# Kernel tuning notes

Measured on AMD Instinct MI355X. Metric: run time of the kernel, lower is better.

The kernel has to match this reference:

```python
import jax, jax.numpy as jnp
import numpy as np

N_NODES = 100000
N_EDGES = 3200000
N_FEAT = 128
HIDDEN = 16


def gcn_conv(x, W, b, row, col, ew, n):
    """PyG GCNConv: linear -> add self-loops -> sym deg-norm -> scatter-add -> bias."""
    x = x @ W  # [n, out]
    loop = jnp.arange(n)
    row = jnp.concatenate([row, loop])
    col = jnp.concatenate([col, loop])
    ew = jnp.concatenate([ew, jnp.ones((n,), ew.dtype)])  # self-loop weight 1
    deg = jax.ops.segment_sum(ew, col, num_segments=n)  # in-degree by edge weight
    dinv = jnp.where(deg > 0, jax.lax.rsqrt(deg), 0.0)
    norm = dinv[row] * ew * dinv[col]  # [E+n]
    # gather source features, scale, scatter-add at destinations
    out = jax.ops.segment_sum(x[row] * norm[:, None], col, num_segments=n)
    return out + b


def setup_inputs() -> dict:
    key = jax.random.key(0)
    k = jax.random.split(key, 7)
    x = jax.random.normal(k[0], (N_NODES, N_FEAT), dtype=jnp.float32)
    edge_index = jax.random.randint(k[1], (2, N_EDGES), 0, N_NODES, dtype=jnp.int64)
    edge_weight = jax.random.uniform(k[2], (N_EDGES,), dtype=jnp.float32)
    s1 = 1.0 / np.sqrt(N_FEAT)
    s2 = 1.0 / np.sqrt(HIDDEN)
    W1 = jax.random.uniform(k[3], (N_FEAT, HIDDEN), jnp.float32, -s1, s1)
    b1 = jnp.zeros((HIDDEN,), jnp.float32)
    W2 = jax.random.uniform(k[4], (HIDDEN, 1), jnp.float32, -s2, s2)
    b2 = jnp.zeros((1,), jnp.float32)
    return {"x": x, "edge_index": edge_index, "edge_weight": edge_weight,
            "W1": W1, "b1": b1, "W2": W2, "b2": b2}


def reference(x, edge_index, edge_weight, W1, b1, W2, b2):
    n = x.shape[0]
    row, col = edge_index[0], edge_index[1]
    h = gcn_conv(x, W1, b1, row, col, edge_weight, n)
    h = jax.nn.relu(h)
    h = gcn_conv(h, W2, b2, row, col, edge_weight, n)
    return jax.nn.sigmoid(h)[:, 0].astype(jnp.float32)  # squeeze(1)
```

## Files before the change

### kernel.cpp

```cpp
#include <hip/hip_runtime.h>
#include <hip/hip_fp16.h>
#include <math.h>

#define NNODES 100000
#define NEDGES 3200000
#define NF 128
#define NH 16
#define SB 192
#define NSB 521
#define NBLK 512
#define EPB (NEDGES / NBLK)
#define CAP2 6912
#define XWBLK 391

__device__ __forceinline__ __half2 u2h(unsigned u) { union { unsigned u; __half2 h; } c; c.u = u; return c.h; }
__device__ __forceinline__ unsigned h2u(__half2 h) { union { unsigned u; __half2 h; } c; c.h = h; return c.u; }
__device__ __forceinline__ __half2 shfl_h2(__half2 v, int m) {
    int x = __shfl_xor(*(int*)&v, m);
    return *(__half2*)&x;
}

__global__ void k_histxw(const int* __restrict__ col, unsigned* __restrict__ ghist,
                         const float* __restrict__ x, const float* __restrict__ W1,
                         unsigned* __restrict__ xwh) {
    __shared__ float w[NF * NH];
    __shared__ unsigned h[NSB];
    int t = threadIdx.x, b = blockIdx.x;
    if (b < NBLK) {
        for (int i = t; i < NSB; i += 256) h[i] = 0u;
        __syncthreads();
        const int2* c2 = (const int2*)(col + b * EPB);
        for (int i = t; i < EPB / 2; i += 256) {
            int2 c = c2[i];
            atomicAdd(&h[(unsigned)c.x / SB], 1u);
            atomicAdd(&h[(unsigned)c.y / SB], 1u);
        }
        __syncthreads();
        for (int i = t; i < NSB; i += 256) ghist[(size_t)b * NSB + i] = h[i];
    } else {
        for (int i = t; i < NF * NH; i += 256) w[i] = W1[i];
        __syncthreads();
        int i = (b - NBLK) * 256 + t;
        if (i >= NNODES) return;
        float acc[NH];
#pragma unroll
        for (int f = 0; f < NH; ++f) acc[f] = 0.f;
        const float4* xr = (const float4*)(x + (long long)i * NF);
#pragma unroll 8
        for (int k4 = 0; k4 < NF / 4; ++k4) {
            float4 v = xr[k4];
            const float* wk = &w[k4 * 4 * NH];
#pragma unroll
            for (int f = 0; f < NH; ++f)
                acc[f] += v.x * wk[f] + v.y * wk[NH + f] + v.z * wk[2 * NH + f] + v.w * wk[3 * NH + f];
        }
        unsigned u[8];
#pragma unroll
        for (int j = 0; j < 8; ++j)
            u[j] = h2u(__floats2half2_rn(acc[2 * j], acc[2 * j + 1]));
        uint4* o = (uint4*)(xwh + (size_t)i * 8);
        o[0] = make_uint4(u[0], u[1], u[2], u[3]);
        o[1] = make_uint4(u[4], u[5], u[6], u[7]);
    }
}

__global__ __launch_bounds__(NBLK) void k_scan1(unsigned* __restrict__ ghist,
                                                unsigned* __restrict__ totals) {
    int k = blockIdx.x, t = threadIdx.x;
    __shared__ unsigned s[NBLK];
    unsigned v = ghist[(size_t)t * NSB + k];
    s[t] = v;
    __syncthreads();
    for (int off = 1; off < NBLK; off <<= 1) {
        unsigned x = (t >= off) ? s[t - off] : 0u;
        __syncthreads();
        s[t] += x;
        __syncthreads();
    }
    ghist[(size_t)t * NSB + k] = s[t] - v;
    if (t == NBLK - 1) totals[k] = s[t];
}

__global__ __launch_bounds__(512) void k_scatB1(
        const int* __restrict__ row, const int* __restrict__ col,
        const float* __restrict__ ew,
        const unsigned* __restrict__ ghist, const unsigned* __restrict__ totals,
        uint2* __restrict__ spack, unsigned* __restrict__ sbase_out) {
    __shared__ uint2 stage[EPB];
    __shared__ unsigned short sbArr[EPB];
    __shared__ unsigned lcnt[NSB];
    __shared__ unsigned gdelta[NSB];
    __shared__ unsigned scn[512];
    int t = threadIdx.x, b = blockIdx.x;
    int e0 = b * EPB;
    for (int i = t; i < NSB; i += 512) lcnt[i] = 0u;
    __syncthreads();
    const int2* c2 = (const int2*)(col + e0);
    for (int i = t; i < EPB / 2; i += 512) {
        int2 c = c2[i];
        atomicAdd(&lcnt[(unsigned)c.x / SB], 1u);
        atomicAdd(&lcnt[(unsigned)c.y / SB], 1u);
    }
    __syncthreads();
    unsigned tv[2];
    unsigned tp = 0;
#pragma unroll
    for (int j = 0; j < 2; ++j) {
        int i = t * 2 + j;
        tv[j] = (i < NSB) ? totals[i] : 0u;
        tp += tv[j];
    }
    scn[t] = tp;
    __syncthreads();
    for (int off = 1; off < 512; off <<= 1) {
        unsigned x = (t >= off) ? scn[t - off] : 0u;
        __syncthreads();
        scn[t] += x;
        __syncthreads();
    }
    unsigned trun = scn[t] - tp;
    unsigned sb_[2];
#pragma unroll
    for (int j = 0; j < 2; ++j) { sb_[j] = trun; trun += tv[j]; }
    __syncthreads();
    unsigned v[2];
    unsigned p = 0;
#pragma unroll
    for (int j = 0; j < 2; ++j) {
        int i = t * 2 + j;
        v[j] = (i < NSB) ? lcnt[i] : 0u;
        p += v[j];
    }
    scn[t] = p;
    __syncthreads();
    for (int off = 1; off < 512; off <<= 1) {
        unsigned x = (t >= off) ? scn[t - off] : 0u;
        __syncthreads();
        scn[t] += x;
        __syncthreads();
    }
    unsigned run = scn[t] - p;
    __syncthreads();
    unsigned lst[2];
#pragma unroll
    for (int j = 0; j < 2; ++j) {
        int i = t * 2 + j;
        if (i < NSB) {
            lst[j] = run;
            gdelta[i] = sb_[j] + ghist[(size_t)b * NSB + i] - run;
        }
        run += v[j];
    }
    __syncthreads();
#pragma unroll
    for (int j = 0; j < 2; ++j) {
        int i = t * 2 + j;
        if (i < NSB) lcnt[i] = lst[j];
    }
    if (b == 0) {
#pragma unroll
        for (int j = 0; j < 2; ++j) {
            int i = t * 2 + j;
            if (i < NSB) sbase_out[i] = sb_[j];
        }
        if (t == 0) sbase_out[NSB] = NEDGES;
    }
    __syncthreads();
    const int2* r2 = (const int2*)(row + e0);
    const float2* w2 = (const float2*)(ew + e0);
    for (int i = t; i < EPB / 2; i += 512) {
        int2 rr = r2[i];
        int2 cc = c2[i];
        float2 ww = w2[i];
        unsigned sb = (unsigned)cc.x / SB;
        unsigned ln = (unsigned)cc.x - sb * SB;
        unsigned pos = atomicAdd(&lcnt[sb], 1u);
        stage[pos] = make_uint2((unsigned)rr.x | (ln << 17), __float_as_uint(ww.x));
        sbArr[pos] = (unsigned short)sb;
        sb = (unsigned)cc.y / SB;
        ln = (unsigned)cc.y - sb * SB;
        pos = atomicAdd(&lcnt[sb], 1u);
        stage[pos] = make_uint2((unsigned)rr.y | (ln << 17), __float_as_uint(ww.y));
        sbArr[pos] = (unsigned short)sb;
    }
    __syncthreads();
    for (int i = t; i < EPB; i += 512)
        spack[i + gdelta[sbArr[i]]] = stage[i];
}

__global__ __launch_bounds__(512) void k_degdinv(
        const uint2* __restrict__ spack, const unsigned* __restrict__ sbase,
        unsigned* __restrict__ start, float* __restrict__ dinv) {
    __shared__ unsigned hist[SB];
    __shared__ float wdeg[SB];
    __shared__ unsigned scn[512];
    int k = blockIdx.x, t = threadIdx.x;
    unsigned e0 = sbase[k], e1 = sbase[k + 1];
    int ne = (int)(e1 - e0);
    if (t < SB) { hist[t] = 0u; wdeg[t] = 0.f; }
    __syncthreads();
    for (int i = t; i < ne; i += 512) {
        uint2 p = spack[e0 + i];
        unsigned ln = p.x >> 17;
        atomicAdd(&hist[ln], 1u);
        atomicAdd(&wdeg[ln], __uint_as_float(p.y));
    }
    __syncthreads();
    unsigned v = (t < SB) ? hist[t] : 0u;
    scn[t] = v;
    __syncthreads();
    for (int off = 1; off < 512; off <<= 1) {
        unsigned x = (t >= off) ? scn[t - off] : 0u;
        __syncthreads();
        scn[t] += x;
        __syncthreads();
    }
    unsigned excl = scn[t] - v;
    int g = k * SB + t;
    if (t < SB && g < NNODES) {
        start[g] = e0 + excl;
        dinv[g] = rsqrtf(wdeg[t] + 1.0f);
    }
}

__global__ __launch_bounds__(1024) void k_sedge1(
        const uint2* __restrict__ spack, const unsigned* __restrict__ sbase,
        const unsigned* __restrict__ start, const unsigned* __restrict__ xwh,
        const float* __restrict__ dinv, const float* __restrict__ b1,
        const float* __restrict__ W2, float* __restrict__ zn) {
    __shared__ uint2 ed[CAP2];
    __shared__ unsigned lcnt[SB];
    int k = blockIdx.x, t = threadIdx.x;
    unsigned e0 = sbase[k], e1 = sbase[k + 1];
    int ne = (int)(e1 - e0);
    if (t < SB) {
        int g = k * SB + t;
        lcnt[t] = (g < NNODES) ? (start[g] - e0) : (unsigned)ne;
    }
    __syncthreads();
    for (int i = t; i < ne; i += 1024) {
        uint2 p = spack[e0 + i];
        unsigned ln = p.x >> 17;
        unsigned r = p.x & 0x1FFFFu;
        float wd = __uint_as_float(p.y) * dinv[r];
        unsigned pos = atomicAdd(&lcnt[ln], 1u);
        ed[pos] = make_uint2(r, h2u(__float2half2_rn(wd)));
    }
    __syncthreads();
    int wave = t >> 6, lane = t & 63;
    int fg = lane & 3, e4 = lane >> 2;
#pragma unroll
    for (int j = 0; j < SB / 16; ++j) {
        int ln = wave * (SB / 16) + j;
        int g = k * SB + ln;
        if (g >= NNODES) break;
        unsigned o0 = (ln == 0) ? 0u : lcnt[ln - 1];
        unsigned o1 = lcnt[ln];
        __half2 a0 = __float2half2_rn(0.f), a1 = a0;
        for (unsigned e = o0 + e4; e < o1; e += 16) {
            uint2 d = ed[e];
            uint2 q = *(const uint2*)(xwh + (size_t)d.x * 8 + fg * 2);
            a0 = __hfma2(u2h(q.x), u2h(d.y), a0);
            a1 = __hfma2(u2h(q.y), u2h(d.y), a1);
        }
#pragma unroll
        for (int m = 4; m < 64; m <<= 1) {
            a0 = __hadd2(a0, shfl_h2(a0, m));
            a1 = __hadd2(a1, shfl_h2(a1, m));
        }
        float di = dinv[g];
        uint2 qs = *(const uint2*)(xwh + (size_t)g * 8 + fg * 2);
        float ax = __low2float(a0)  + di * __low2float(u2h(qs.x));
        float ay = __high2float(a0) + di * __high2float(u2h(qs.x));
        float az = __low2float(a1)  + di * __low2float(u2h(qs.y));
        float aw = __high2float(a1) + di * __high2float(u2h(qs.y));
        float4 b4 = ((const float4*)b1)[fg];
        float4 w4 = ((const float4*)W2)[fg];
        float s = fmaxf(di * ax + b4.x, 0.f) * w4.x
                + fmaxf(di * ay + b4.y, 0.f) * w4.y
                + fmaxf(di * az + b4.z, 0.f) * w4.z
                + fmaxf(di * aw + b4.w, 0.f) * w4.w;
        s += __shfl_xor(s, 1);
        s += __shfl_xor(s, 2);
        if (lane == 0) zn[g] = s * di;
    }
}

__global__ __launch_bounds__(512) void k_edge2acc(
        const uint2* __restrict__ spack, const unsigned* __restrict__ sbase,
        const float* __restrict__ zn, const float* __restrict__ dinv,
        const float* __restrict__ b2, float* __restrict__ out) {
    __shared__ float zacc[SB];
    int k = blockIdx.x, t = threadIdx.x;
    if (t < SB) zacc[t] = 0.f;
    __syncthreads();
    unsigned e0 = sbase[k], e1 = sbase[k + 1];
    for (unsigned e = e0 + t; e < e1; e += 512) {
        uint2 p = spack[e];
        atomicAdd(&zacc[p.x >> 17], zn[p.x & 0x1FFFFu] * __uint_as_float(p.y));
    }
    __syncthreads();
    int g = k * SB + t;
    if (t < SB && g < NNODES) {
        float di = dinv[g];
        float v = di * zacc[t] + di * zn[g] + b2[0];
        out[g] = 1.f / (1.f + expf(-v));
    }
}

extern "C" void kernel_launch(void* const* d_in, const int* in_sizes, int n_in,
                              void* d_out, int out_size, void* d_ws, size_t ws_size,
                              hipStream_t stream) {
    const float* x  = (const float*)d_in[0];
    const int* eidx = (const int*)d_in[1];
    const float* ew = (const float*)d_in[2];
    const float* W1 = (const float*)d_in[3];
    const float* b1 = (const float*)d_in[4];
    const float* W2 = (const float*)d_in[5];
    const float* b2 = (const float*)d_in[6];
    float* out = (float*)d_out;

    const int* row = eidx;
    const int* col = eidx + NEDGES;

    unsigned* ws = (unsigned*)d_ws;
    uint2*    spack  = (uint2*)ws;
    unsigned* xwh    = ws + 6400000;
    float*    dinv   = (float*)(ws + 7200000);
    float*    zn     = (float*)(ws + 7300000);
    unsigned* start  = ws + 7400000;
    unsigned* sbase  = ws + 7500000;
    unsigned* totals = ws + 7500522;
    unsigned* ghist  = ws + 7501043;

    k_histxw <<<NBLK + XWBLK, 256, 0, stream>>>(col, ghist, x, W1, xwh);
    k_scan1  <<<NSB, NBLK, 0, stream>>>(ghist, totals);
    k_scatB1 <<<NBLK, 512, 0, stream>>>(row, col, ew, ghist, totals, spack, sbase);
    k_degdinv<<<NSB, 512, 0, stream>>>(spack, sbase, start, dinv);
    k_sedge1 <<<NSB, 1024, 0, stream>>>(spack, sbase, start, xwh, dinv, b1, W2, zn);
    k_edge2acc<<<NSB, 512, 0, stream>>>(spack, sbase, zn, dinv, b2, out);
}
```

Before: 145.9 us.

## Store bucketed edges as split row/fp16-weight arrays and prescale XW by dinv

```diff
diff --git a/kernel.cpp b/kernel.cpp
--- a/kernel.cpp
+++ b/kernel.cpp
@@ -19,6 +19,9 @@
     int x = __shfl_xor(*(int*)&v, m);
     return *(__half2*)&x;
 }
+__device__ __forceinline__ unsigned f2h(float f) {
+    return h2u(__floats2half2_rn(f, 0.f)) & 0xffffu;
+}
 
 __global__ void k_histxw(const int* __restrict__ col, unsigned* __restrict__ ghist,
                          const float* __restrict__ x, const float* __restrict__ W1,
@@ -85,8 +88,10 @@
         const int* __restrict__ row, const int* __restrict__ col,
         const float* __restrict__ ew,
         const unsigned* __restrict__ ghist, const unsigned* __restrict__ totals,
-        uint2* __restrict__ spack, unsigned* __restrict__ sbase_out) {
-    __shared__ uint2 stage[EPB];
+        unsigned* __restrict__ brow, unsigned short* __restrict__ bw,
+        unsigned* __restrict__ sbase_out) {
+    __shared__ unsigned stage_row[EPB];
+    __shared__ unsigned short stage_w[EPB];
     __shared__ unsigned short sbArr[EPB];
     __shared__ unsigned lcnt[NSB];
     __shared__ unsigned gdelta[NSB];
@@ -175,41 +180,49 @@
         unsigned sb = (unsigned)cc.x / SB;
         unsigned ln = (unsigned)cc.x - sb * SB;
         unsigned pos = atomicAdd(&lcnt[sb], 1u);
-        stage[pos] = make_uint2((unsigned)rr.x | (ln << 17), __float_as_uint(ww.x));
+        stage_row[pos] = (unsigned)rr.x | (ln << 17);
+        stage_w[pos] = (unsigned short)f2h(ww.x);
         sbArr[pos] = (unsigned short)sb;
         sb = (unsigned)cc.y / SB;
         ln = (unsigned)cc.y - sb * SB;
         pos = atomicAdd(&lcnt[sb], 1u);
-        stage[pos] = make_uint2((unsigned)rr.y | (ln << 17), __float_as_uint(ww.y));
+        stage_row[pos] = (unsigned)rr.y | (ln << 17);
+        stage_w[pos] = (unsigned short)f2h(ww.y);
         sbArr[pos] = (unsigned short)sb;
     }
     __syncthreads();
-    for (int i = t; i < EPB; i += 512)
-        spack[i + gdelta[sbArr[i]]] = stage[i];
-}
-
-__global__ __launch_bounds__(512) void k_degdinv(
-        const uint2* __restrict__ spack, const unsigned* __restrict__ sbase,
-        unsigned* __restrict__ start, float* __restrict__ dinv) {
+    for (int i = t; i < EPB; i += 512) {
+        unsigned pos = i + gdelta[sbArr[i]];
+        brow[pos] = stage_row[i];
+        bw[pos] = stage_w[i];
+    }
+}
+
+__global__ __launch_bounds__(1024) void k_degdinv(
+        const unsigned* __restrict__ brow, const unsigned short* __restrict__ bw,
+        const unsigned* __restrict__ sbase,
+        unsigned* __restrict__ start, float* __restrict__ dinv,
+        const unsigned* __restrict__ xwh, unsigned* __restrict__ xwn) {
     __shared__ unsigned hist[SB];
     __shared__ float wdeg[SB];
-    __shared__ unsigned scn[512];
+    __shared__ unsigned scn[1024];
     int k = blockIdx.x, t = threadIdx.x;
     unsigned e0 = sbase[k], e1 = sbase[k + 1];
     int ne = (int)(e1 - e0);
     if (t < SB) { hist[t] = 0u; wdeg[t] = 0.f; }
     __syncthreads();
-    for (int i = t; i < ne; i += 512) {
-        uint2 p = spack[e0 + i];
-        unsigned ln = p.x >> 17;
+    for (int i = t; i < ne; i += 1024) {
+        unsigned p = brow[e0 + i];
+        unsigned wu = bw[e0 + i];
+        unsigned ln = p >> 17;
         atomicAdd(&hist[ln], 1u);
-        atomicAdd(&wdeg[ln], __uint_as_float(p.y));
+        atomicAdd(&wdeg[ln], __low2float(u2h(wu)));
     }
     __syncthreads();
     unsigned v = (t < SB) ? hist[t] : 0u;
     scn[t] = v;
     __syncthreads();
-    for (int off = 1; off < 512; off <<= 1) {
+    for (int off = 1; off < 1024; off <<= 1) {
         unsigned x = (t >= off) ? scn[t - off] : 0u;
         __syncthreads();
         scn[t] += x;
@@ -219,16 +232,34 @@
     int g = k * SB + t;
     if (t < SB && g < NNODES) {
         start[g] = e0 + excl;
-        dinv[g] = rsqrtf(wdeg[t] + 1.0f);
+        float di = rsqrtf(wdeg[t] + 1.0f);
+        dinv[g] = di;
+        __half2 d2 = __float2half2_rn(di);
+        const uint4* xi = (const uint4*)(xwh + (size_t)g * 8);
+        uint4 A = xi[0], B = xi[1];
+        uint4 o0, o1;
+        o0.x = h2u(__hmul2(u2h(A.x), d2));
+        o0.y = h2u(__hmul2(u2h(A.y), d2));
+        o0.z = h2u(__hmul2(u2h(A.z), d2));
+        o0.w = h2u(__hmul2(u2h(A.w), d2));
+        o1.x = h2u(__hmul2(u2h(B.x), d2));
+        o1.y = h2u(__hmul2(u2h(B.y), d2));
+        o1.z = h2u(__hmul2(u2h(B.z), d2));
+        o1.w = h2u(__hmul2(u2h(B.w), d2));
+        uint4* o = (uint4*)(xwn + (size_t)g * 8);
+        o[0] = o0;
+        o[1] = o1;
     }
 }
 
 __global__ __launch_bounds__(1024) void k_sedge1(
-        const uint2* __restrict__ spack, const unsigned* __restrict__ sbase,
-        const unsigned* __restrict__ start, const unsigned* __restrict__ xwh,
+        const unsigned* __restrict__ brow, const unsigned short* __restrict__ bw,
+        const unsigned* __restrict__ sbase,
+        const unsigned* __restrict__ start, const unsigned* __restrict__ xwn,
         const float* __restrict__ dinv, const float* __restrict__ b1,
         const float* __restrict__ W2, float* __restrict__ zn) {
-    __shared__ uint2 ed[CAP2];
+    __shared__ unsigned ed_row[CAP2];
+    __shared__ unsigned short ed_w[CAP2];
     __shared__ unsigned lcnt[SB];
     int k = blockIdx.x, t = threadIdx.x;
     unsigned e0 = sbase[k], e1 = sbase[k + 1];
@@ -239,12 +270,12 @@
     }
     __syncthreads();
     for (int i = t; i < ne; i += 1024) {
-        uint2 p = spack[e0 + i];
-        unsigned ln = p.x >> 17;
-        unsigned r = p.x & 0x1FFFFu;
-        float wd = __uint_as_float(p.y) * dinv[r];
+        unsigned p = brow[e0 + i];
+        unsigned short wu = bw[e0 + i];
+        unsigned ln = p >> 17;
         unsigned pos = atomicAdd(&lcnt[ln], 1u);
-        ed[pos] = make_uint2(r, h2u(__float2half2_rn(wd)));
+        ed_row[pos] = p & 0x1FFFFu;
+        ed_w[pos] = wu;
     }
     __syncthreads();
     int wave = t >> 6, lane = t & 63;
@@ -258,22 +289,23 @@
         unsigned o1 = lcnt[ln];
         __half2 a0 = __float2half2_rn(0.f), a1 = a0;
         for (unsigned e = o0 + e4; e < o1; e += 16) {
-            uint2 d = ed[e];
-            uint2 q = *(const uint2*)(xwh + (size_t)d.x * 8 + fg * 2);
-            a0 = __hfma2(u2h(q.x), u2h(d.y), a0);
-            a1 = __hfma2(u2h(q.y), u2h(d.y), a1);
+            unsigned r = ed_row[e];
+            unsigned ww = (unsigned)ed_w[e] * 0x10001u;
+            uint2 q = *(const uint2*)(xwn + (size_t)r * 8 + fg * 2);
+            a0 = __hfma2(u2h(q.x), u2h(ww), a0);
+            a1 = __hfma2(u2h(q.y), u2h(ww), a1);
         }
 #pragma unroll
         for (int m = 4; m < 64; m <<= 1) {
             a0 = __hadd2(a0, shfl_h2(a0, m));
             a1 = __hadd2(a1, shfl_h2(a1, m));
         }
+        float ax = __low2float(a0), ay = __high2float(a0);
+        float az = __low2float(a1), aw = __high2float(a1);
+        uint2 qs = *(const uint2*)(xwn + (size_t)g * 8 + fg * 2);
+        ax += __low2float(u2h(qs.x)); ay += __high2float(u2h(qs.x));
+        az += __low2float(u2h(qs.y)); aw += __high2float(u2h(qs.y));
         float di = dinv[g];
-        uint2 qs = *(const uint2*)(xwh + (size_t)g * 8 + fg * 2);
-        float ax = __low2float(a0)  + di * __low2float(u2h(qs.x));
-        float ay = __high2float(a0) + di * __high2float(u2h(qs.x));
-        float az = __low2float(a1)  + di * __low2float(u2h(qs.y));
-        float aw = __high2float(a1) + di * __high2float(u2h(qs.y));
         float4 b4 = ((const float4*)b1)[fg];
         float4 w4 = ((const float4*)W2)[fg];
         float s = fmaxf(di * ax + b4.x, 0.f) * w4.x
@@ -287,7 +319,8 @@
 }
 
 __global__ __launch_bounds__(512) void k_edge2acc(
-        const uint2* __restrict__ spack, const unsigned* __restrict__ sbase,
+        const unsigned* __restrict__ brow, const unsigned short* __restrict__ bw,
+        const unsigned* __restrict__ sbase,
         const float* __restrict__ zn, const float* __restrict__ dinv,
         const float* __restrict__ b2, float* __restrict__ out) {
     __shared__ float zacc[SB];
@@ -296,8 +329,9 @@
     __syncthreads();
     unsigned e0 = sbase[k], e1 = sbase[k + 1];
     for (unsigned e = e0 + t; e < e1; e += 512) {
-        uint2 p = spack[e];
-        atomicAdd(&zacc[p.x >> 17], zn[p.x & 0x1FFFFu] * __uint_as_float(p.y));
+        unsigned p = brow[e];
+        float w = __low2float(u2h((unsigned)bw[e]));
+        atomicAdd(&zacc[p >> 17], zn[p & 0x1FFFFu] * w);
     }
     __syncthreads();
     int g = k * SB + t;
@@ -324,19 +358,21 @@
     const int* col = eidx + NEDGES;
 
     unsigned* ws = (unsigned*)d_ws;
-    uint2*    spack  = (uint2*)ws;
-    unsigned* xwh    = ws + 6400000;
-    float*    dinv   = (float*)(ws + 7200000);
-    float*    zn     = (float*)(ws + 7300000);
-    unsigned* start  = ws + 7400000;
-    unsigned* sbase  = ws + 7500000;
-    unsigned* totals = ws + 7500522;
-    unsigned* ghist  = ws + 7501043;
+    unsigned*       brow   = ws;
+    unsigned short* bw     = (unsigned short*)(ws + 3200000);
+    unsigned*       xwh    = ws + 4800000;
+    unsigned*       xwn    = ws + 5600000;
+    float*          dinv   = (float*)(ws + 6400000);
+    float*          zn     = (float*)(ws + 6500000);
+    unsigned*       start  = ws + 6600000;
+    unsigned*       sbase  = ws + 6700000;
+    unsigned*       totals = ws + 6700522;
+    unsigned*       ghist  = ws + 6701043;
 
     k_histxw <<<NBLK + XWBLK, 256, 0, stream>>>(col, ghist, x, W1, xwh);
     k_scan1  <<<NSB, NBLK, 0, stream>>>(ghist, totals);
-    k_scatB1 <<<NBLK, 512, 0, stream>>>(row, col, ew, ghist, totals, spack, sbase);
-    k_degdinv<<<NSB, 512, 0, stream>>>(spack, sbase, start, dinv);
-    k_sedge1 <<<NSB, 1024, 0, stream>>>(spack, sbase, start, xwh, dinv, b1, W2, zn);
-    k_edge2acc<<<NSB, 512, 0, stream>>>(spack, sbase, zn, dinv, b2, out);
-}
+    k_scatB1 <<<NBLK, 512, 0, stream>>>(row, col, ew, ghist, totals, brow, bw, sbase);
+    k_degdinv<<<NSB, 1024, 0, stream>>>(brow, bw, sbase, start, dinv, xwh, xwn);
+    k_sedge1 <<<NSB, 1024, 0, stream>>>(brow, bw, sbase, start, xwn, dinv, b1, W2, zn);
+    k_edge2acc<<<NSB, 512, 0, stream>>>(brow, bw, sbase, zn, dinv, b2, out);
+}
```

Measured after the change: 138.4 us. -5.1%, faster.
